# Kernel optimization log

Hardware: AMD Instinct MI355X
Metric: run time of the kernel (lower is better)

The kernel has to match this reference:

```python
import jax, jax.numpy as jnp
import numpy as np

N_UNITS = 1024
D_K = 64
B, S = 4, 2048
NEG = 1.0e9


def setup_inputs() -> dict:
    key = jax.random.key(0)
    ks = jax.random.split(key, 11)
    k = float(np.sqrt(1.0 / N_UNITS))
    u = lambda kk, shape: jax.random.uniform(kk, shape, jnp.float32, -k, k)
    Q = jax.random.normal(ks[0], (B, S, N_UNITS), jnp.float32)
    K = jax.random.normal(ks[1], (B, S, N_UNITS), jnp.float32)
    V = jax.random.normal(ks[2], (B, S, N_UNITS), jnp.float32)
    mask = jax.random.randint(ks[3], (B, S, S), 0, 2, jnp.int32)
    return {
        "Q": Q, "K": K, "V": V, "mask": mask,
        "Wq_w": u(ks[4], (D_K, N_UNITS)), "Wq_b": u(ks[5], (D_K,)),
        "Wk_w": u(ks[6], (D_K, N_UNITS)), "Wk_b": u(ks[7], (D_K,)),
        "Wv_w": u(ks[8], (D_K, N_UNITS)), "Wv_b": u(ks[9], (D_K,)),
    }


def reference(Q, K, V, mask, Wq_w, Wq_b, Wk_w, Wk_b, Wv_w, Wv_b):
    # Linear projections (torch Linear: x @ W.T + b)
    Q_ = jnp.einsum('bsu,du->bsd', Q, Wq_w) + Wq_b  # [B,S,D_K]
    K_ = jnp.einsum('bsu,du->bsd', K, Wk_w) + Wk_b
    V_ = jnp.einsum('bsu,du->bsd', V, Wv_w) + Wv_b
    scores = jnp.einsum('bid,bjd->bij', Q_, K_) / jnp.sqrt(jnp.float32(D_K))
    m = mask.astype(jnp.float32)
    # custom multiplicative-additive mask: scores*mask - 1e9*(1-mask)
    masked = scores * m - NEG * (1.0 - m)
    attn = jax.nn.softmax(masked, axis=-1)
    # dropout p=0.0 -> identity
    return jnp.einsum('bij,bjd->bid', attn, V_)
```

## Files before the change

### kernel.cpp

```cpp
#include <hip/hip_runtime.h>
#include <stdint.h>

#define S_ 2048

typedef __bf16 bf16x8 __attribute__((ext_vector_type(8)));
typedef float f32x4 __attribute__((ext_vector_type(4)));
typedef unsigned int u32x4 __attribute__((ext_vector_type(4)));

union FragU { u32x4 u; bf16x8 v; unsigned short s[8]; };

__device__ __forceinline__ unsigned short f2bf(float f) {
    unsigned int u = __builtin_bit_cast(unsigned int, f);
    u += 0x7fffu + ((u >> 16) & 1u);
    return (unsigned short)(u >> 16);
}

__device__ __forceinline__ unsigned int pk2(float a, float b) {
    return (unsigned int)f2bf(a) | ((unsigned int)f2bf(b) << 16);
}

__global__ __launch_bounds__(256, 4) void proj_kernel(
    const float* __restrict__ Q, const float* __restrict__ K, const float* __restrict__ V,
    const float* __restrict__ Wq, const float* __restrict__ Wk, const float* __restrict__ Wv,
    const float* __restrict__ Bq, const float* __restrict__ Bk, const float* __restrict__ Bv,
    unsigned short* __restrict__ Qb, unsigned short* __restrict__ Kb,
    unsigned short* __restrict__ Vt)
{
    const int tid = threadIdx.x;
    const int w = tid >> 6, lane = tid & 63;
    const int lm = lane & 15, quad = lane >> 4;
    const int mat = blockIdx.y;
    const int row0 = blockIdx.x * 16;

    __shared__ unsigned short Xs[16][1032];

    const float* X    = (mat == 0) ? Q  : (mat == 1) ? K  : V;
    const float* W    = (mat == 0) ? Wq : (mat == 1) ? Wk : Wv;
    const float* Bias = (mat == 0) ? Bq : (mat == 1) ? Bk : Bv;

    #pragma unroll 4
    for (int p = 0; p < 16; ++p) {
        float4 xv = *(const float4*)(X + (row0 + p) * 1024 + tid * 4);
        uint2 xb;
        xb.x = pk2(xv.x, xv.y);
        xb.y = pk2(xv.z, xv.w);
        *(uint2*)&Xs[p][tid * 4] = xb;
    }
    __syncthreads();

    const int col = w * 16 + lm;
    const float* wrow = W + col * 1024;
    f32x4 acc = {0.f, 0.f, 0.f, 0.f};

    #pragma unroll 4
    for (int s = 0; s < 16; ++s) {
        const int k0 = s * 64;
        FragU af0, af1, bf0, bf1;
        af0.u = *(const u32x4*)&Xs[lm][k0 + quad * 8];
        af1.u = *(const u32x4*)&Xs[lm][k0 + 32 + quad * 8];
        float4 w0 = *(const float4*)(wrow + k0 + quad * 8);
        float4 w1 = *(const float4*)(wrow + k0 + quad * 8 + 4);
        float4 w2 = *(const float4*)(wrow + k0 + 32 + quad * 8);
        float4 w3 = *(const float4*)(wrow + k0 + 32 + quad * 8 + 4);
        bf0.u[0] = pk2(w0.x, w0.y); bf0.u[1] = pk2(w0.z, w0.w);
        bf0.u[2] = pk2(w1.x, w1.y); bf0.u[3] = pk2(w1.z, w1.w);
        bf1.u[0] = pk2(w2.x, w2.y); bf1.u[1] = pk2(w2.z, w2.w);
        bf1.u[2] = pk2(w3.x, w3.y); bf1.u[3] = pk2(w3.z, w3.w);
        acc = __builtin_amdgcn_mfma_f32_16x16x32_bf16(af0.v, bf0.v, acc, 0, 0, 0);
        acc = __builtin_amdgcn_mfma_f32_16x16x32_bf16(af1.v, bf1.v, acc, 0, 0, 0);
    }

    const float bias = Bias[col];
    if (mat == 2) {
        ushort4 vv;
        unsigned short* vs = (unsigned short*)&vv;
        #pragma unroll
        for (int r = 0; r < 4; ++r) vs[r] = f2bf(acc[r] + bias);
        *(ushort4*)&Vt[(row0 >> 11) * 131072 + col * 2048 + (row0 & 2047) + quad * 4] = vv;
    } else {
        unsigned short* dst = (mat == 0) ? Qb : Kb;
        #pragma unroll
        for (int r = 0; r < 4; ++r)
            dst[(row0 + quad * 4 + r) * 64 + col] = f2bf(acc[r] + bias);
    }
}

__global__ __launch_bounds__(512) void attn_kernel(
    const unsigned short* __restrict__ Qb, const unsigned short* __restrict__ Kb,
    const unsigned short* __restrict__ Vt, const int* __restrict__ mask,
    float* __restrict__ out)
{
    const int tid = threadIdx.x;
    const int w = tid >> 6, lane = tid & 63;
    const int lm = lane & 15, quad = lane >> 4;
    const int q0 = blockIdx.x * 16;
    const int b = blockIdx.y;

    __shared__ unsigned long long Mb[16][32];
    __shared__ unsigned short Plds[8][16 * 72];
    __shared__ float Olds[8][1024];
    __shared__ float llds[8][16];

    const int* mrow = mask + (b * 2048 + q0) * 2048;
    #pragma unroll 2
    for (int p = 0; p < 16; ++p) {
        int m0 = mrow[p * 2048 + tid];
        int m1 = mrow[p * 2048 + tid + 512];
        int m2 = mrow[p * 2048 + tid + 1024];
        int m3 = mrow[p * 2048 + tid + 1536];
        unsigned long long b0 = __ballot(m0 != 0);
        unsigned long long b1 = __ballot(m1 != 0);
        unsigned long long b2 = __ballot(m2 != 0);
        unsigned long long b3 = __ballot(m3 != 0);
        if (lane == 0) {
            Mb[p][w]      = b0;
            Mb[p][w + 8]  = b1;
            Mb[p][w + 16] = b2;
            Mb[p][w + 24] = b3;
        }
    }

    FragU qf0, qf1;
    const unsigned short* qptr = Qb + (b * 2048 + q0 + lm) * 64 + quad * 8;
    qf0.u = *(const u32x4*)qptr;
    qf1.u = *(const u32x4*)(qptr + 32);

    f32x4 o[4];
    #pragma unroll
    for (int dt = 0; dt < 4; ++dt) { f32x4 z = {0.f,0.f,0.f,0.f}; o[dt] = z; }
    float lsum[4] = {0.f, 0.f, 0.f, 0.f};

    const unsigned short* kbase = Kb + b * 2048 * 64;
    const unsigned short* vbase = Vt + b * 131072;

    __syncthreads();

    #pragma unroll
    for (int iter = 0; iter < 4; ++iter) {
        const int k0 = w * 256 + iter * 64;
        const int kw = k0 >> 6;

        f32x4 sc[4];
        #pragma unroll
        for (int ct = 0; ct < 4; ++ct) {
            const unsigned short* kptr = kbase + (k0 + ct * 16 + lm) * 64 + quad * 8;
            FragU kf0, kf1;
            kf0.u = *(const u32x4*)kptr;
            kf1.u = *(const u32x4*)(kptr + 32);
            f32x4 a = {0.f,0.f,0.f,0.f};
            a = __builtin_amdgcn_mfma_f32_16x16x32_bf16(qf0.v, kf0.v, a, 0, 0, 0);
            a = __builtin_amdgcn_mfma_f32_16x16x32_bf16(qf1.v, kf1.v, a, 0, 0, 0);
            sc[ct] = a;
        }

        unsigned long long mb[4];
        #pragma unroll
        for (int r = 0; r < 4; ++r) mb[r] = Mb[quad * 4 + r][kw];

        #pragma unroll
        for (int ct = 0; ct < 4; ++ct) {
            #pragma unroll
            for (int r = 0; r < 4; ++r) {
                float p = ((mb[r] >> (ct * 16 + lm)) & 1ull)
                          ? __expf(sc[ct][r] * 0.125f) : 0.f;
                sc[ct][r] = p;
                lsum[r] += p;
            }
        }

        #pragma unroll
        for (int ct = 0; ct < 4; ++ct)
            #pragma unroll
            for (int r = 0; r < 4; ++r)
                Plds[w][(quad * 4 + r) * 72 + ct * 16 + lm] = f2bf(sc[ct][r]);

        #pragma unroll
        for (int ks = 0; ks < 2; ++ks) {
            FragU pf;
            pf.u = *(const u32x4*)&Plds[w][lm * 72 + ks * 32 + quad * 8];
            #pragma unroll
            for (int dt = 0; dt < 4; ++dt) {
                FragU vf;
                vf.u = *(const u32x4*)(vbase + (dt * 16 + lm) * 2048 + k0 + ks * 32 + quad * 8);
                o[dt] = __builtin_amdgcn_mfma_f32_16x16x32_bf16(pf.v, vf.v, o[dt], 0, 0, 0);
            }
        }
    }

    #pragma unroll
    for (int r = 0; r < 4; ++r)
        #pragma unroll
        for (int off = 1; off <= 8; off <<= 1)
            lsum[r] += __shfl_xor(lsum[r], off, 64);

    #pragma unroll
    for (int dt = 0; dt < 4; ++dt)
        #pragma unroll
        for (int r = 0; r < 4; ++r)
            Olds[w][(quad * 4 + r) * 64 + dt * 16 + lm] = o[dt][r];
    if (lm == 0)
        #pragma unroll
        for (int r = 0; r < 4; ++r) llds[w][quad * 4 + r] = lsum[r];
    __syncthreads();

    #pragma unroll
    for (int i = 0; i < 2; ++i) {
        int e = i * 512 + tid;
        int q = e >> 6, d = e & 63;
        float L = 0.f, val = 0.f;
        #pragma unroll
        for (int ww = 0; ww < 8; ++ww) {
            L   += llds[ww][q];
            val += Olds[ww][q * 64 + d];
        }
        out[(b * 2048 + q0 + q) * 64 + d] = val / L;
    }
}

extern "C" void kernel_launch(void* const* d_in, const int* in_sizes, int n_in,
                              void* d_out, int out_size, void* d_ws, size_t ws_size,
                              hipStream_t stream) {
    const float* Q   = (const float*)d_in[0];
    const float* K   = (const float*)d_in[1];
    const float* V   = (const float*)d_in[2];
    const int* mask  = (const int*)d_in[3];
    const float* Wq  = (const float*)d_in[4];
    const float* bq  = (const float*)d_in[5];
    const float* Wk  = (const float*)d_in[6];
    const float* bk  = (const float*)d_in[7];
    const float* Wv  = (const float*)d_in[8];
    const float* bv  = (const float*)d_in[9];
    float* out = (float*)d_out;

    char* ws = (char*)d_ws;
    unsigned short* Qb = (unsigned short*)(ws);
    unsigned short* Kb = (unsigned short*)(ws + (1u << 20));
    unsigned short* Vt = (unsigned short*)(ws + (2u << 20));

    hipLaunchKernelGGL(proj_kernel, dim3(512, 3), dim3(256), 0, stream,
                       Q, K, V, Wq, Wk, Wv, bq, bk, bv, Qb, Kb, Vt);
    hipLaunchKernelGGL(attn_kernel, dim3(128, 4), dim3(512), 0, stream,
                       Qb, Kb, Vt, mask, out);
}
```

Before: 254.3 us.

## Pre-pack weights and mask bits, load X via direct LDS, fragment-order V

Adds a small kernel that converts the projection weights to bf16 once, in MFMA fragment order, so each projection block stops re-reading and converting fp32 weights. A separate kernel packs the int mask into bitmasks, and the attention kernel now reads those bits instead of the full int32 mask. The projection kernel stages fp32 X straight into LDS with global_load_lds and converts it to bf16 at fragment load time. V is stored in fragment-contiguous order so each attention lane issues one coalesced 16-byte load. The cost is two extra kernel launches and a larger LDS footprint in the projection kernel, which now allows 2 blocks per CU instead of 4.

```diff
diff --git a/kernel.cpp b/kernel.cpp
--- a/kernel.cpp
+++ b/kernel.cpp
@@ -14,17 +14,55 @@
     u += 0x7fffu + ((u >> 16) & 1u);
     return (unsigned short)(u >> 16);
 }
-
 __device__ __forceinline__ unsigned int pk2(float a, float b) {
     return (unsigned int)f2bf(a) | ((unsigned int)f2bf(b) << 16);
 }
-
-__global__ __launch_bounds__(256, 4) void proj_kernel(
+__device__ __forceinline__ void gl_lds16(const void* g, void* l) {
+    __builtin_amdgcn_global_load_lds(
+        (const __attribute__((address_space(1))) unsigned int*)g,
+        (__attribute__((address_space(3))) unsigned int*)l, 16, 0, 0);
+}
+
+__global__ __launch_bounds__(256) void cvt_w_kernel(
+    const float* __restrict__ wq, const float* __restrict__ wk,
+    const float* __restrict__ wv, u32x4* __restrict__ Wt4)
+{
+    const int lane = threadIdx.x & 63;
+    const int lm = lane & 15, quad = lane >> 4;
+    const int f = blockIdx.x * 4 + (threadIdx.x >> 6);
+    const int mat = f >> 7, cg = (f >> 5) & 3, s = f & 31;
+    const float* W = (mat == 0) ? wq : (mat == 1) ? wk : wv;
+    const float* src = W + (cg * 16 + lm) * 1024 + s * 32 + quad * 8;
+    float4 a = *(const float4*)(src);
+    float4 b = *(const float4*)(src + 4);
+    FragU o;
+    o.u[0] = pk2(a.x, a.y); o.u[1] = pk2(a.z, a.w);
+    o.u[2] = pk2(b.x, b.y); o.u[3] = pk2(b.z, b.w);
+    Wt4[f * 64 + lane] = o.u;
+}
+
+__global__ __launch_bounds__(256) void mask_pack(
+    const int* __restrict__ mask, unsigned long long* __restrict__ bits)
+{
+    const int lane = threadIdx.x & 63;
+    const int wid = (blockIdx.x * 256 + threadIdx.x) >> 6;
+    const int* p = mask + wid * 512 + lane;
+    int m[8];
+    #pragma unroll
+    for (int j = 0; j < 8; ++j) m[j] = p[j * 64];
+    #pragma unroll
+    for (int j = 0; j < 8; ++j) {
+        unsigned long long b = __ballot(m[j] != 0);
+        if (lane == 0) bits[wid * 8 + j] = b;
+    }
+}
+
+__global__ __launch_bounds__(256, 2) void proj_kernel(
     const float* __restrict__ Q, const float* __restrict__ K, const float* __restrict__ V,
-    const float* __restrict__ Wq, const float* __restrict__ Wk, const float* __restrict__ Wv,
+    const u32x4* __restrict__ Wt4,
     const float* __restrict__ Bq, const float* __restrict__ Bk, const float* __restrict__ Bv,
     unsigned short* __restrict__ Qb, unsigned short* __restrict__ Kb,
-    unsigned short* __restrict__ Vt)
+    unsigned short* __restrict__ Vf)
 {
     const int tid = threadIdx.x;
     const int w = tid >> 6, lane = tid & 63;
@@ -32,51 +70,51 @@
     const int mat = blockIdx.y;
     const int row0 = blockIdx.x * 16;
 
-    __shared__ unsigned short Xs[16][1032];
+    __shared__ __align__(16) float Xs[16][1028];
 
     const float* X    = (mat == 0) ? Q  : (mat == 1) ? K  : V;
-    const float* W    = (mat == 0) ? Wq : (mat == 1) ? Wk : Wv;
     const float* Bias = (mat == 0) ? Bq : (mat == 1) ? Bk : Bv;
 
-    #pragma unroll 4
-    for (int p = 0; p < 16; ++p) {
-        float4 xv = *(const float4*)(X + (row0 + p) * 1024 + tid * 4);
-        uint2 xb;
-        xb.x = pk2(xv.x, xv.y);
-        xb.y = pk2(xv.z, xv.w);
-        *(uint2*)&Xs[p][tid * 4] = xb;
+    {
+        const int rbase = w * 4;
+        #pragma unroll
+        for (int i = 0; i < 16; ++i) {
+            const int r = rbase + (i >> 2);
+            const int qd = i & 3;
+            gl_lds16(X + (row0 + r) * 1024 + qd * 256 + lane * 4,
+                     &Xs[r][qd * 256]);
+        }
     }
     __syncthreads();
 
+    f32x4 acc = {0.f, 0.f, 0.f, 0.f};
+    const u32x4* wfrag = Wt4 + (mat * 128 + w * 32) * 64 + lane;
+    #pragma unroll 8
+    for (int s = 0; s < 32; ++s) {
+        f32x4 a0 = *(const f32x4*)&Xs[lm][s * 32 + quad * 8];
+        f32x4 a1 = *(const f32x4*)&Xs[lm][s * 32 + quad * 8 + 4];
+        FragU af, bfr;
+        af.u[0] = pk2(a0[0], a0[1]); af.u[1] = pk2(a0[2], a0[3]);
+        af.u[2] = pk2(a1[0], a1[1]); af.u[3] = pk2(a1[2], a1[3]);
+        bfr.u = wfrag[s * 64];
+        acc = __builtin_amdgcn_mfma_f32_16x16x32_bf16(af.v, bfr.v, acc, 0, 0, 0);
+    }
+
     const int col = w * 16 + lm;
-    const float* wrow = W + col * 1024;
-    f32x4 acc = {0.f, 0.f, 0.f, 0.f};
-
-    #pragma unroll 4
-    for (int s = 0; s < 16; ++s) {
-        const int k0 = s * 64;
-        FragU af0, af1, bf0, bf1;
-        af0.u = *(const u32x4*)&Xs[lm][k0 + quad * 8];
-        af1.u = *(const u32x4*)&Xs[lm][k0 + 32 + quad * 8];
-        float4 w0 = *(const float4*)(wrow + k0 + quad * 8);
-        float4 w1 = *(const float4*)(wrow + k0 + quad * 8 + 4);
-        float4 w2 = *(const float4*)(wrow + k0 + 32 + quad * 8);
-        float4 w3 = *(const float4*)(wrow + k0 + 32 + quad * 8 + 4);
-        bf0.u[0] = pk2(w0.x, w0.y); bf0.u[1] = pk2(w0.z, w0.w);
-        bf0.u[2] = pk2(w1.x, w1.y); bf0.u[3] = pk2(w1.z, w1.w);
-        bf1.u[0] = pk2(w2.x, w2.y); bf1.u[1] = pk2(w2.z, w2.w);
-        bf1.u[2] = pk2(w3.x, w3.y); bf1.u[3] = pk2(w3.z, w3.w);
-        acc = __builtin_amdgcn_mfma_f32_16x16x32_bf16(af0.v, bf0.v, acc, 0, 0, 0);
-        acc = __builtin_amdgcn_mfma_f32_16x16x32_bf16(af1.v, bf1.v, acc, 0, 0, 0);
-    }
-
     const float bias = Bias[col];
     if (mat == 2) {
+        const int seq0 = row0 + quad * 4;
+        const int b_ = seq0 >> 11;
+        const int s = seq0 & 2047;
+        const int sb = s >> 5, s32 = s & 31;
+        const int fq = s32 >> 3, j0 = s32 & 7;
         ushort4 vv;
         unsigned short* vs = (unsigned short*)&vv;
         #pragma unroll
         for (int r = 0; r < 4; ++r) vs[r] = f2bf(acc[r] + bias);
-        *(ushort4*)&Vt[(row0 >> 11) * 131072 + col * 2048 + (row0 & 2047) + quad * 4] = vv;
+        char* dst = (char*)Vf + ((b_ * 64 + sb) * 4 + w) * 1024
+                    + (fq * 16 + lm) * 16 + j0 * 2;
+        *(ushort4*)dst = vv;
     } else {
         unsigned short* dst = (mat == 0) ? Qb : Kb;
         #pragma unroll
@@ -87,7 +125,7 @@
 
 __global__ __launch_bounds__(512) void attn_kernel(
     const unsigned short* __restrict__ Qb, const unsigned short* __restrict__ Kb,
-    const unsigned short* __restrict__ Vt, const int* __restrict__ mask,
+    const u32x4* __restrict__ Vf4, const unsigned long long* __restrict__ bits,
     float* __restrict__ out)
 {
     const int tid = threadIdx.x;
@@ -101,23 +139,9 @@
     __shared__ float Olds[8][1024];
     __shared__ float llds[8][16];
 
-    const int* mrow = mask + (b * 2048 + q0) * 2048;
-    #pragma unroll 2
-    for (int p = 0; p < 16; ++p) {
-        int m0 = mrow[p * 2048 + tid];
-        int m1 = mrow[p * 2048 + tid + 512];
-        int m2 = mrow[p * 2048 + tid + 1024];
-        int m3 = mrow[p * 2048 + tid + 1536];
-        unsigned long long b0 = __ballot(m0 != 0);
-        unsigned long long b1 = __ballot(m1 != 0);
-        unsigned long long b2 = __ballot(m2 != 0);
-        unsigned long long b3 = __ballot(m3 != 0);
-        if (lane == 0) {
-            Mb[p][w]      = b0;
-            Mb[p][w + 8]  = b1;
-            Mb[p][w + 16] = b2;
-            Mb[p][w + 24] = b3;
-        }
+    {
+        const int p = tid >> 5, kw = tid & 31;
+        Mb[p][kw] = bits[(b * 2048 + q0 + p) * 32 + kw];
     }
 
     FragU qf0, qf1;
@@ -131,7 +155,7 @@
     float lsum[4] = {0.f, 0.f, 0.f, 0.f};
 
     const unsigned short* kbase = Kb + b * 2048 * 64;
-    const unsigned short* vbase = Vt + b * 131072;
+    const u32x4* vbase = Vf4 + (b * 64) * 4 * 64;
 
     __syncthreads();
 
@@ -178,10 +202,11 @@
         for (int ks = 0; ks < 2; ++ks) {
             FragU pf;
             pf.u = *(const u32x4*)&Plds[w][lm * 72 + ks * 32 + quad * 8];
+            const int sb = (k0 >> 5) + ks;
             #pragma unroll
             for (int dt = 0; dt < 4; ++dt) {
                 FragU vf;
-                vf.u = *(const u32x4*)(vbase + (dt * 16 + lm) * 2048 + k0 + ks * 32 + quad * 8);
+                vf.u = vbase[(sb * 4 + dt) * 64 + lane];
                 o[dt] = __builtin_amdgcn_mfma_f32_16x16x32_bf16(pf.v, vf.v, o[dt], 0, 0, 0);
             }
         }
@@ -235,10 +260,14 @@
     char* ws = (char*)d_ws;
     unsigned short* Qb = (unsigned short*)(ws);
     unsigned short* Kb = (unsigned short*)(ws + (1u << 20));
-    unsigned short* Vt = (unsigned short*)(ws + (2u << 20));
-
+    unsigned short* Vf = (unsigned short*)(ws + (2u << 20));
+    u32x4* Wt4 = (u32x4*)(ws + (3u << 20));
+    unsigned long long* bits = (unsigned long long*)(ws + (4u << 20));
+
+    hipLaunchKernelGGL(cvt_w_kernel, dim3(96), dim3(256), 0, stream, Wq, Wk, Wv, Wt4);
+    hipLaunchKernelGGL(mask_pack, dim3(8192), dim3(256), 0, stream, mask, bits);
     hipLaunchKernelGGL(proj_kernel, dim3(512, 3), dim3(256), 0, stream,
-                       Q, K, V, Wq, Wk, Wv, bq, bk, bv, Qb, Kb, Vt);
+                       Q, K, V, Wt4, bq, bk, bv, Qb, Kb, Vf);
     hipLaunchKernelGGL(attn_kernel, dim3(128, 4), dim3(512), 0, stream,
-                       Qb, Kb, Vt, mask, out);
-}
+                       Qb, Kb, (const u32x4*)Vf, bits, out);
+}
```

Measured after the change: 217.0 us. -14.7%, faster.
